# Kernel optimization log

Measured on AMD Instinct MI355X. Metric: run time of the kernel, lower is better.

## Reference

```python
import jax, jax.numpy as jnp
import numpy as np

D = 768       # GATv2 in/out feats (num_heads=1)
D_OUT = 384   # fc output
K = 51        # round(top_rate * L) = round(0.1 * 512)
EPS = 1e-5    # nn.LayerNorm default eps


def _layer_norm(x, g, b):
    mu = jnp.mean(x, axis=-1, keepdims=True)
    var = jnp.mean((x - mu) ** 2, axis=-1, keepdims=True)
    return (x - mu) / jnp.sqrt(var + EPS) * g + b


def setup_inputs() -> dict:
    key = jax.random.key(0)
    ks = jax.random.split(key, 12)
    B, L = 4, 512
    s = 0.02
    return {
        "hidden_state": jax.random.normal(ks[0], (B, L, D), jnp.float32),
        "attention": jax.random.uniform(ks[1], (B, L, L), jnp.float32),
        # GATv2Conv params (fc_src, fc_dst, attn vector, output bias)
        "W_src": jax.random.normal(ks[2], (D, D), jnp.float32) * s,
        "b_src": jnp.zeros((D,), jnp.float32),
        "W_dst": jax.random.normal(ks[3], (D, D), jnp.float32) * s,
        "b_dst": jnp.zeros((D,), jnp.float32),
        "attn_vec": jax.random.normal(ks[4], (D,), jnp.float32) * s,
        "gat_bias": jnp.zeros((D,), jnp.float32),
        # GlobalAttentionPooling gate_nn: Linear(768, 1)
        "gate_W": jax.random.normal(ks[5], (D, 1), jnp.float32) * s,
        "gate_b": jnp.zeros((1,), jnp.float32),
        # LayerNorm(768)
        "ln_g": jnp.ones((D,), jnp.float32),
        "ln_b": jnp.zeros((D,), jnp.float32),
        # fc: Linear(768, 384)
        "fc_W": jax.random.normal(ks[6], (D, D_OUT), jnp.float32) * s,
        "fc_b": jnp.zeros((D_OUT,), jnp.float32),
        # LayerNorm(384)
        "ln2_g": jnp.ones((D_OUT,), jnp.float32),
        "ln2_b": jnp.zeros((D_OUT,), jnp.float32),
        "mask": jnp.ones((B, L), jnp.int32),  # unused by the original forward
        "type": 0,                              # unused string/type flag
    }


def reference(hidden_state, attention, W_src, b_src, W_dst, b_dst, attn_vec,
              gat_bias, gate_W, gate_b, ln_g, ln_b, fc_W, fc_b, ln2_g, ln2_b,
              mask, type):
    B, L, _ = hidden_state.shape
    # --- topk sparsification: each node i keeps K source neighbors ---
    vals, idx = jax.lax.top_k(attention, K)          # [B, L, K]
    valid = vals > 0.0                                # edges kept by pos_sign filter

    # --- GATv2Conv (num_heads=1, residual=Identity since 768==768) ---
    feat_src = hidden_state @ W_src + b_src           # [B, L, D]
    feat_dst = hidden_state @ W_dst + b_dst           # [B, L, D]
    g = feat_src[jnp.arange(B)[:, None, None], idx]   # [B, L, K, D] gathered src feats
    e = jax.nn.leaky_relu(g + feat_dst[:, :, None, :], 0.2)
    scores = jnp.einsum("blkd,d->blk", e, attn_vec)   # [B, L, K]
    scores = jnp.where(valid, scores, -1e9)           # removed edges masked out
    a = jax.nn.softmax(scores, axis=-1)               # edge_softmax per dst node
    h = jnp.einsum("blk,blkd->bld", a, g)             # weighted scatter-sum
    h = h + hidden_state + gat_bias                   # residual (identity) + bias
    h = jax.nn.leaky_relu(h, 0.01)                    # nn.LeakyReLU activation

    # --- GlobalAttentionPooling: softmax(gate) weighted segment reduce ---
    gate = h @ gate_W + gate_b                        # [B, L, 1]
    p = jax.nn.softmax(gate, axis=1)
    pooled = jnp.sum(p * h, axis=1)                   # [B, D]

    # --- head: fc(dropout(ln(relu(out)))) then ln2 (dropout = eval identity) ---
    out = _layer_norm(jax.nn.relu(pooled), ln_g, ln_b)
    out = out @ fc_W + fc_b
    out = _layer_norm(out, ln2_g, ln2_b)
    return out
```

## Files before the change

kernel.cpp:

```cpp
#include <hip/hip_runtime.h>
#include <math.h>

#define D 768
#define DOUT 384
#define LSEQ 512
#define BATCH 4
#define KTOP 51
#define EPS 1e-5f

typedef unsigned short ushort_t;
typedef __bf16 bf16x8 __attribute__((ext_vector_type(8)));
typedef float f32x4 __attribute__((ext_vector_type(4)));

#define GLOAD16(gp, lp)                                                        \
    __builtin_amdgcn_global_load_lds(                                          \
        (const __attribute__((address_space(1))) unsigned int*)(gp),           \
        (__attribute__((address_space(3))) unsigned int*)(lp), 16, 0, 0)

__device__ __forceinline__ ushort_t f2bf(float f) {
    unsigned int u = __builtin_bit_cast(unsigned int, f);
    u = (u + 0x7FFFu + ((u >> 16) & 1u)) >> 16;
    return (ushort_t)u;
}

__device__ __forceinline__ float bf2f(ushort_t u) {
    unsigned int v = ((unsigned int)u) << 16;
    return __builtin_bit_cast(float, v);
}

__global__ __launch_bounds__(256) void prep_kernel(const float* __restrict__ hidden,
                                                   ushort_t* __restrict__ Ah,
                                                   const float* __restrict__ W0,
                                                   const float* __restrict__ W1,
                                                   ushort_t* __restrict__ WT0,
                                                   ushort_t* __restrict__ WT1,
                                                   float* __restrict__ pooled,
                                                   float* __restrict__ z) {
    __shared__ float tile[32][33];
    const int bid = blockIdx.x;
    const int tid = threadIdx.x;
    if (bid < 1536) {
        const int i = (bid * 256 + tid) * 4;
        const float4 v = *(const float4*)(hidden + i);
        ushort4 o;
        o.x = f2bf(v.x); o.y = f2bf(v.y); o.z = f2bf(v.z); o.w = f2bf(v.w);
        *(ushort4*)(Ah + i) = o;
    } else if (bid < 2688) {
        const int t = bid - 1536;
        const int zz = t / 576;
        const int rem = t - zz * 576;
        const int by = rem / 24, bx = rem - by * 24;
        const float* W = zz ? W1 : W0;
        ushort_t* WT = zz ? WT1 : WT0;
        const int kbase = by * 32;
        const int nbase = bx * 32;
        const int r = tid >> 3, c4 = (tid & 7) * 4;

        const float4 v = *(const float4*)(W + (size_t)(kbase + r) * D + nbase + c4);
        tile[r][c4 + 0] = v.x; tile[r][c4 + 1] = v.y;
        tile[r][c4 + 2] = v.z; tile[r][c4 + 3] = v.w;
        __syncthreads();
        ushort4 o;
        o.x = f2bf(tile[c4 + 0][r]); o.y = f2bf(tile[c4 + 1][r]);
        o.z = f2bf(tile[c4 + 2][r]); o.w = f2bf(tile[c4 + 3][r]);
        *(ushort4*)(WT + (size_t)(nbase + r) * D + kbase + c4) = o;
    } else {
        for (int i = tid; i < BATCH * D; i += 256) pooled[i] = 0.f;
        for (int i = tid; i < BATCH * DOUT; i += 256) z[i] = 0.f;
    }
}

__global__ __launch_bounds__(256) void feat_gemm_kernel(const ushort_t* __restrict__ Ah,
                                                        const ushort_t* __restrict__ WT0,
                                                        const float* __restrict__ b0,
                                                        ushort_t* __restrict__ Csrc_bf,
                                                        const ushort_t* __restrict__ WT1,
                                                        const float* __restrict__ b1,
                                                        float* __restrict__ Cdst) {
    const ushort_t* WT = blockIdx.z ? WT1 : WT0;
    const float* bias = blockIdx.z ? b1 : b0;

    __shared__ ushort_t As[64 * 32];
    __shared__ ushort_t Bs[64 * 32];

    const int tid = threadIdx.x;
    const int lane = tid & 63;
    const int wave = tid >> 6;
    const int quad = lane >> 4;
    const int m15 = lane & 15;
    const int qRow = (wave & 1) * 32;
    const int qCol = (wave >> 1) * 32;

    const int rowBase = blockIdx.y * 64;
    const int colBase = blockIdx.x * 64;

    const int e0 = tid * 8;
    const int r0 = e0 >> 5;
    const int c0 = e0 & 31;
    const ushort_t* Abase = Ah + (size_t)rowBase * D;
    const ushort_t* Bbase = WT + (size_t)colBase * D;

    f32x4 acc[2][2] = {};

    for (int kk = 0; kk < D; kk += 32) {
        __syncthreads();
        GLOAD16(Abase + (size_t)r0 * D + kk + c0, &As[e0]);
        GLOAD16(Bbase + (size_t)r0 * D + kk + c0, &Bs[e0]);
        __syncthreads();

        bf16x8 a[2], b[2];
#pragma unroll
        for (int i = 0; i < 2; ++i)
            a[i] = *(const bf16x8*)&As[(qRow + i * 16 + m15) * 32 + quad * 8];
#pragma unroll
        for (int j = 0; j < 2; ++j)
            b[j] = *(const bf16x8*)&Bs[(qCol + j * 16 + m15) * 32 + quad * 8];
#pragma unroll
        for (int i = 0; i < 2; ++i)
#pragma unroll
            for (int j = 0; j < 2; ++j)
                acc[i][j] = __builtin_amdgcn_mfma_f32_16x16x32_bf16(a[i], b[j], acc[i][j], 0, 0, 0);
    }

    if (blockIdx.z == 0) {
#pragma unroll
        for (int j = 0; j < 2; ++j) {
            const int col = colBase + qCol + j * 16 + m15;
            const float bv = bias[col];
#pragma unroll
            for (int i = 0; i < 2; ++i) {
                ushort_t* Cp = Csrc_bf + (size_t)(rowBase + qRow + i * 16 + quad * 4) * D + col;
#pragma unroll
                for (int r = 0; r < 4; ++r)
                    Cp[(size_t)r * D] = f2bf(acc[i][j][r] + bv);
            }
        }
    } else {
#pragma unroll
        for (int j = 0; j < 2; ++j) {
            const int col = colBase + qCol + j * 16 + m15;
            const float bv = bias[col];
#pragma unroll
            for (int i = 0; i < 2; ++i) {
                float* Cp = Cdst + (size_t)(rowBase + qRow + i * 16 + quad * 4) * D + col;
#pragma unroll
                for (int r = 0; r < 4; ++r)
                    Cp[(size_t)r * D] = acc[i][j][r] + bv;
            }
        }
    }
}

__global__ __launch_bounds__(256) void transpose_fsrc_kernel(const ushort_t* __restrict__ I,
                                                             ushort_t* __restrict__ O) {
    __shared__ ushort_t tile[32][33];
    const int b = blockIdx.z;
    const int cbase = blockIdx.x * 32;
    const int rbase = blockIdx.y * 32;
    const int tid = threadIdx.x;
    const int tr = tid >> 3, tc4 = (tid & 7) * 4;

    const ushort_t* Ib = I + (size_t)b * LSEQ * D;
    ushort_t* Ob = O + (size_t)b * D * LSEQ;

    const ushort4 v = *(const ushort4*)(Ib + (size_t)(rbase + tr) * D + cbase + tc4);
    tile[tr][tc4 + 0] = v.x; tile[tr][tc4 + 1] = v.y;
    tile[tr][tc4 + 2] = v.z; tile[tr][tc4 + 3] = v.w;
    __syncthreads();
    ushort4 o;
    o.x = tile[tc4 + 0][tr]; o.y = tile[tc4 + 1][tr];
    o.z = tile[tc4 + 2][tr]; o.w = tile[tc4 + 3][tr];
    *(ushort4*)(Ob + (size_t)(cbase + tr) * LSEQ + rbase + tc4) = o;
}

__global__ __launch_bounds__(256) void score_kernel(const float* __restrict__ attn,
                                                    const ushort_t* __restrict__ fsrc_bf,
                                                    const float* __restrict__ feat_dst,
                                                    const float* __restrict__ attn_vec,
                                                    const float* __restrict__ gate_b,
                                                    ushort_t* __restrict__ P,
                                                    float* __restrict__ gate) {
    const int row = blockIdx.x;
    const int b = row >> 9;
    const int tid = threadIdx.x;
    const int lane = tid & 63;
    const int wave = tid >> 6;

    __shared__ float vals[LSEQ];
    __shared__ float cval[320];
    __shared__ int   cidx[320];
    __shared__ int   nhi, outSlot;
    __shared__ float sc[KTOP];
    __shared__ int   kid[KTOP];
    __shared__ float kvv[KTOP];

    ((unsigned int*)(P + (size_t)row * LSEQ))[tid] = 0u;
    if (tid == 0) { gate[row] = gate_b[0]; nhi = 0; outSlot = 0; }

    const float* a = attn + (size_t)row * LSEQ;
    const float v0 = a[tid];
    const float v1 = a[tid + 256];
    vals[tid] = v0;
    vals[tid + 256] = v1;
    __syncthreads();

    if (v0 > 0.75f) {
        const int s = atomicAdd(&nhi, 1);
        if (s < 320) { cval[s] = v0; cidx[s] = tid; }
    }
    if (v1 > 0.75f) {
        const int s = atomicAdd(&nhi, 1);
        if (s < 320) { cval[s] = v1; cidx[s] = tid + 256; }
    }
    __syncthreads();

    const int n = nhi;
    if (n >= KTOP && n <= 320) {
        if (tid < n) {
            const float v = cval[tid];
            const int e = cidx[tid];
            int r = 0;
            for (int j = 0; j < n; ++j) {
                const float u = cval[j];
                r += (u > v) || (u == v && cidx[j] < e);
            }
            if (r < KTOP) {
                const int s = atomicAdd(&outSlot, 1);
                kid[s] = e; kvv[s] = v;
            }
        }
    } else {
#pragma unroll
        for (int e0 = 0; e0 < 2; ++e0) {
            const int e = tid + e0 * 256;
            const float v = vals[e];
            int r = 0;
            for (int j = 0; j < LSEQ; ++j) {
                const float u = vals[j];
                r += (u > v) || (u == v && j < e);
            }
            if (r < KTOP) {
                const int s = atomicAdd(&outSlot, 1);
                kid[s] = e; kvv[s] = v;
            }
        }
    }

    const float* fdp = feat_dst + (size_t)row * D;
    float fdr[16], avr[16];
    {
        const int d0 = lane * 8;
        const float4 f0 = *(const float4*)(fdp + d0);
        const float4 f1 = *(const float4*)(fdp + d0 + 4);
        const float4 a0 = *(const float4*)(attn_vec + d0);
        const float4 a1 = *(const float4*)(attn_vec + d0 + 4);
        fdr[0]=f0.x; fdr[1]=f0.y; fdr[2]=f0.z; fdr[3]=f0.w;
        fdr[4]=f1.x; fdr[5]=f1.y; fdr[6]=f1.z; fdr[7]=f1.w;
        avr[0]=a0.x; avr[1]=a0.y; avr[2]=a0.z; avr[3]=a0.w;
        avr[4]=a1.x; avr[5]=a1.y; avr[6]=a1.z; avr[7]=a1.w;
    }
    if (lane < 32) {
        const int d1 = (lane + 64) * 8;
        const float4 f0 = *(const float4*)(fdp + d1);
        const float4 f1 = *(const float4*)(fdp + d1 + 4);
        const float4 a0 = *(const float4*)(attn_vec + d1);
        const float4 a1 = *(const float4*)(attn_vec + d1 + 4);
        fdr[8]=f0.x; fdr[9]=f0.y; fdr[10]=f0.z; fdr[11]=f0.w;
        fdr[12]=f1.x; fdr[13]=f1.y; fdr[14]=f1.z; fdr[15]=f1.w;
        avr[8]=a0.x; avr[9]=a0.y; avr[10]=a0.z; avr[11]=a0.w;
        avr[12]=a1.x; avr[13]=a1.y; avr[14]=a1.z; avr[15]=a1.w;
    }
    __syncthreads();

    for (int k = wave; k < KTOP; k += 4) {
        const ushort_t* g = fsrc_bf + ((size_t)(b << 9) + kid[k]) * D;
        float s = 0.f;
        const bf16x8 g0 = *(const bf16x8*)(g + lane * 8);
#pragma unroll
        for (int jj = 0; jj < 8; ++jj) {
            float x = (float)g0[jj] + fdr[jj];
            x = x > 0.f ? x : 0.2f * x;
            s += x * avr[jj];
        }
        if (lane < 32) {
            const bf16x8 g1 = *(const bf16x8*)(g + (lane + 64) * 8);
#pragma unroll
            for (int jj = 0; jj < 8; ++jj) {
                float x = (float)g1[jj] + fdr[8 + jj];
                x = x > 0.f ? x : 0.2f * x;
                s += x * avr[8 + jj];
            }
        }
#pragma unroll
        for (int off = 32; off > 0; off >>= 1) s += __shfl_down(s, off);
        if (lane == 0) sc[k] = (kvv[k] > 0.f) ? s : -1e9f;
    }
    __syncthreads();

    if (wave == 0) {
        float s = (lane < KTOP) ? sc[lane] : -3.0e38f;
        float m = s;
#pragma unroll
        for (int off = 32; off > 0; off >>= 1) m = fmaxf(m, __shfl_xor(m, off));
        float e = (lane < KTOP) ? __expf(s - m) : 0.f;
        float sum = e;
#pragma unroll
        for (int off = 32; off > 0; off >>= 1) sum += __shfl_xor(sum, off);
        if (lane < KTOP) sc[lane] = e / sum;
    }
    __syncthreads();

    if (tid < KTOP)
        P[(size_t)row * LSEQ + kid[tid]] = f2bf(sc[tid]);
}

__global__ __launch_bounds__(256) void pgemm_kernel(const ushort_t* __restrict__ P,
                                                    const ushort_t* __restrict__ fsrcT,
                                                    const float* __restrict__ gat_bias,
                                                    const float* __restrict__ hidden,
                                                    const float* __restrict__ gate_W,
                                                    ushort_t* __restrict__ h,
                                                    float* __restrict__ gate) {
    const int bb = blockIdx.z;
    const ushort_t* Ab = P + (size_t)bb * LSEQ * LSEQ;
    const ushort_t* Bb = fsrcT + (size_t)bb * D * LSEQ;

    __shared__ ushort_t As[64 * 32];
    __shared__ ushort_t Bs[64 * 32];

    const int tid = threadIdx.x;
    const int lane = tid & 63;
    const int wave = tid >> 6;
    const int quad = lane >> 4;
    const int m15 = lane & 15;
    const int qRow = (wave & 1) * 32;
    const int qCol = (wave >> 1) * 32;

    const int rowBase = blockIdx.y * 64;
    const int colBase = blockIdx.x * 64;

    const int e0 = tid * 8;
    const int r0 = e0 >> 5;
    const int c0 = e0 & 31;
    const ushort_t* Abase = Ab + (size_t)rowBase * LSEQ;
    const ushort_t* Bbase = Bb + (size_t)colBase * LSEQ;

    f32x4 acc[2][2] = {};

    for (int kk = 0; kk < LSEQ; kk += 32) {
        __syncthreads();
        GLOAD16(Abase + (size_t)r0 * LSEQ + kk + c0, &As[e0]);
        GLOAD16(Bbase + (size_t)r0 * LSEQ + kk + c0, &Bs[e0]);
        __syncthreads();

        bf16x8 a[2], b[2];
#pragma unroll
        for (int i = 0; i < 2; ++i)
            a[i] = *(const bf16x8*)&As[(qRow + i * 16 + m15) * 32 + quad * 8];
#pragma unroll
        for (int j = 0; j < 2; ++j)
            b[j] = *(const bf16x8*)&Bs[(qCol + j * 16 + m15) * 32 + quad * 8];
#pragma unroll
        for (int i = 0; i < 2; ++i)
#pragma unroll
            for (int j = 0; j < 2; ++j)
                acc[i][j] = __builtin_amdgcn_mfma_f32_16x16x32_bf16(a[i], b[j], acc[i][j], 0, 0, 0);
    }

    const float* hidb = hidden + (size_t)bb * LSEQ * D;
    ushort_t* hb = h + (size_t)bb * LSEQ * D;
    float rp[2][4] = {};
#pragma unroll
    for (int j = 0; j < 2; ++j) {
        const int col = colBase + qCol + j * 16 + m15;
        const float bv = gat_bias[col];
        const float gw = gate_W[col];
#pragma unroll
        for (int i = 0; i < 2; ++i) {
            const int row0 = rowBase + qRow + i * 16 + quad * 4;
#pragma unroll
            for (int r = 0; r < 4; ++r) {
                float v = acc[i][j][r] + bv + hidb[(size_t)(row0 + r) * D + col];
                v = v > 0.f ? v : 0.01f * v;
                hb[(size_t)(row0 + r) * D + col] = f2bf(v);
                rp[i][r] += v * gw;
            }
        }
    }
#pragma unroll
    for (int i = 0; i < 2; ++i)
#pragma unroll
        for (int r = 0; r < 4; ++r) {
            float p4 = rp[i][r];
            p4 += __shfl_xor(p4, 1);
            p4 += __shfl_xor(p4, 2);
            p4 += __shfl_xor(p4, 4);
            p4 += __shfl_xor(p4, 8);
            if (m15 == 0)
                atomicAdd(&gate[bb * LSEQ + rowBase + qRow + i * 16 + quad * 4 + r], p4);
        }
}

__global__ __launch_bounds__(256) void pool_kernel(const ushort_t* __restrict__ h,
                                                   const float* __restrict__ gate,
                                                   float* __restrict__ pooled) {
    const int b = blockIdx.z;
    const int lbase = blockIdx.y * 64;
    const int d = blockIdx.x * 256 + threadIdx.x;
    const int tid = threadIdx.x;

    __shared__ float red[256];
    __shared__ float ps[64];

    const float g0 = gate[b * LSEQ + tid];
    const float g1 = gate[b * LSEQ + tid + 256];
    red[tid] = fmaxf(g0, g1);
    __syncthreads();
    for (int s = 128; s > 0; s >>= 1) { if (tid < s) red[tid] = fmaxf(red[tid], red[tid + s]); __syncthreads(); }
    const float m = red[0];
    __syncthreads();
    red[tid] = __expf(g0 - m) + __expf(g1 - m);
    __syncthreads();
    for (int s = 128; s > 0; s >>= 1) { if (tid < s) red[tid] += red[tid + s]; __syncthreads(); }
    const float inv = 1.f / red[0];
    if (tid < 64) ps[tid] = __expf(gate[b * LSEQ + lbase + tid] - m) * inv;
    __syncthreads();

    const ushort_t* hb = h + ((size_t)(b * LSEQ + lbase)) * D + d;
    float acc = 0.f;
#pragma unroll 8
    for (int l = 0; l < 64; ++l) {
        acc += ps[l] * bf2f(hb[(size_t)l * D]);
    }
    atomicAdd(&pooled[b * D + d], acc);
}

__global__ __launch_bounds__(256) void fc_kernel(const float* __restrict__ pooled,
                                                 const float* __restrict__ ln_g,
                                                 const float* __restrict__ ln_b,
                                                 const float* __restrict__ fc_W,
                                                 float* __restrict__ z) {
    const int b = blockIdx.z;
    const int by = blockIdx.y;
    const int dbase = by * 256;
    const int jbase = blockIdx.x * 64;
    const int tid = threadIdx.x;
    const int jt = tid & 63;
    const int sub = tid >> 6;

    __shared__ float red[256];
    __shared__ float ys[256];
    __shared__ float part[4][64];

    float v[3];
#pragma unroll
    for (int i = 0; i < 3; ++i) v[i] = fmaxf(pooled[b * D + tid + i * 256], 0.f);

    red[tid] = v[0] + v[1] + v[2];
    __syncthreads();
    for (int s = 128; s > 0; s >>= 1) { if (tid < s) red[tid] += red[tid + s]; __syncthreads(); }
    const float mu = red[0] / (float)D;
    __syncthreads();
    float vs = 0.f;
#pragma unroll
    for (int i = 0; i < 3; ++i) { const float dd = v[i] - mu; vs += dd * dd; }
    red[tid] = vs;
    __syncthreads();
    for (int s = 128; s > 0; s >>= 1) { if (tid < s) red[tid] += red[tid + s]; __syncthreads(); }
    const float rstd = rsqrtf(red[0] / (float)D + EPS);

    const float vb = (by == 0) ? v[0] : (by == 1 ? v[1] : v[2]);
    ys[tid] = (vb - mu) * rstd * ln_g[dbase + tid] + ln_b[dbase + tid];
    __syncthreads();

    const float* W = fc_W + (size_t)(dbase + sub * 64) * DOUT + jbase + jt;
    const float* yy = ys + sub * 64;
    float acc = 0.f;
#pragma unroll 8
    for (int i = 0; i < 64; ++i) {
        acc += yy[i] * W[(size_t)i * DOUT];
    }
    part[sub][jt] = acc;
    __syncthreads();
    if (sub == 0) {
        const float tot = part[0][jt] + part[1][jt] + part[2][jt] + part[3][jt];
        atomicAdd(&z[b * DOUT + jbase + jt], tot);
    }
}

__global__ __launch_bounds__(384) void ln2_kernel(const float* __restrict__ z,
                                                  const float* __restrict__ fc_b,
                                                  const float* __restrict__ ln2_g,
                                                  const float* __restrict__ ln2_b,
                                                  float* __restrict__ out) {
    const int b = blockIdx.x;
    const int tid = threadIdx.x;
    const int lane = tid & 63;
    const int wave = tid >> 6;
    __shared__ float wred[6];

    const float v = z[b * DOUT + tid] + fc_b[tid];

    float s = v;
#pragma unroll
    for (int off = 32; off > 0; off >>= 1) s += __shfl_xor(s, off);
    if (lane == 0) wred[wave] = s;
    __syncthreads();
    float mu = 0.f;
#pragma unroll
    for (int w = 0; w < 6; ++w) mu += wred[w];
    mu /= (float)DOUT;
    __syncthreads();

    const float dd = v - mu;
    float s2 = dd * dd;
#pragma unroll
    for (int off = 32; off > 0; off >>= 1) s2 += __shfl_xor(s2, off);
    if (lane == 0) wred[wave] = s2;
    __syncthreads();
    float var = 0.f;
#pragma unroll
    for (int w = 0; w < 6; ++w) var += wred[w];
    const float rstd = rsqrtf(var / (float)DOUT + EPS);

    out[b * DOUT + tid] = dd * rstd * ln2_g[tid] + ln2_b[tid];
}

extern "C" void kernel_launch(void* const* d_in, const int* in_sizes, int n_in,
                              void* d_out, int out_size, void* d_ws, size_t ws_size,
                              hipStream_t stream) {
    const float* hidden   = (const float*)d_in[0];
    const float* attention= (const float*)d_in[1];
    const float* W_src    = (const float*)d_in[2];
    const float* b_src    = (const float*)d_in[3];
    const float* W_dst    = (const float*)d_in[4];
    const float* b_dst    = (const float*)d_in[5];
    const float* attn_vec = (const float*)d_in[6];
    const float* gat_bias = (const float*)d_in[7];
    const float* gate_W   = (const float*)d_in[8];
    const float* gate_b   = (const float*)d_in[9];
    const float* ln_g     = (const float*)d_in[10];
    const float* ln_b     = (const float*)d_in[11];
    const float* fc_W     = (const float*)d_in[12];
    const float* fc_b     = (const float*)d_in[13];
    const float* ln2_g    = (const float*)d_in[14];
    const float* ln2_b    = (const float*)d_in[15];
    float* out = (float*)d_out;

    const int M = BATCH * LSEQ;
    float* feat_dst = (float*)d_ws;
    float* gate     = feat_dst + (size_t)M * D;
    float* pooled   = gate + M;
    float* z        = pooled + BATCH * D;
    ushort_t* Ah    = (ushort_t*)(z + BATCH * DOUT);
    ushort_t* WT0   = Ah + (size_t)M * D;
    ushort_t* WT1   = WT0 + (size_t)D * D;
    ushort_t* fsrcb = WT1 + (size_t)D * D;
    ushort_t* fsrcT = fsrcb + (size_t)M * D;
    ushort_t* P     = fsrcT + (size_t)M * D;
    ushort_t* h     = P + (size_t)M * LSEQ;

    hipLaunchKernelGGL(prep_kernel, dim3(2689), dim3(256), 0, stream,
                       hidden, Ah, W_src, W_dst, WT0, WT1, pooled, z);
    hipLaunchKernelGGL(feat_gemm_kernel, dim3(D / 64, M / 64, 2), dim3(256), 0, stream,
                       Ah, WT0, b_src, fsrcb, WT1, b_dst, feat_dst);
    hipLaunchKernelGGL(transpose_fsrc_kernel, dim3(D / 32, LSEQ / 32, BATCH), dim3(256), 0, stream,
                       fsrcb, fsrcT);
    hipLaunchKernelGGL(score_kernel, dim3(M), dim3(256), 0, stream,
                       attention, fsrcb, feat_dst, attn_vec, gate_b, P, gate);
    hipLaunchKernelGGL(pgemm_kernel, dim3(D / 64, LSEQ / 64, BATCH), dim3(256), 0, stream,
                       P, fsrcT, gat_bias, hidden, gate_W, h, gate);
    hipLaunchKernelGGL(pool_kernel, dim3(D / 256, LSEQ / 64, BATCH), dim3(256), 0, stream,
                       h, gate, pooled);
    hipLaunchKernelGGL(fc_kernel, dim3(DOUT / 64, D / 256, BATCH), dim3(256), 0, stream,
                       pooled, ln_g, ln_b, fc_W, z);
    hipLaunchKernelGGL(ln2_kernel, dim3(BATCH), dim3(384), 0, stream,
                       z, fc_b, ln2_g, ln2_b, out);
}
```

Measured before the change: 176.6 us.

## Replace dense P-GEMM aggregation with sparse top-k gather kernel and swizzle feat GEMM

The edge aggregation used to scatter softmax weights into a dense 512x512 bf16 P matrix per batch, transpose feat_src, and run a dense GEMM. It now stores the 51 (prob, index) pairs per row and uses a per-row wave gather kernel that sums the weighted bf16 source rows directly and fuses residual, bias, LeakyReLU and the gate dot. This removes the transpose kernel, the P zeroing, the dense GEMM and the gate atomics. The feature GEMM also moves to a 64-wide K tile with an XOR-swizzled LDS layout, and the block reductions in the pool and fc kernels switch to wave shuffles. The gather does irregular row reads that depend on L2 hit rates.

```diff
diff --git a/kernel.cpp b/kernel.cpp
--- a/kernel.cpp
+++ b/kernel.cpp
@@ -80,8 +80,8 @@
     const ushort_t* WT = blockIdx.z ? WT1 : WT0;
     const float* bias = blockIdx.z ? b1 : b0;
 
-    __shared__ ushort_t As[64 * 32];
-    __shared__ ushort_t Bs[64 * 32];
+    __shared__ ushort_t As[64 * 64];
+    __shared__ ushort_t Bs[64 * 64];
 
     const int tid = threadIdx.x;
     const int lane = tid & 63;
@@ -95,31 +95,47 @@
     const int colBase = blockIdx.x * 64;
 
     const int e0 = tid * 8;
-    const int r0 = e0 >> 5;
-    const int c0 = e0 & 31;
+    const int r0 = e0 >> 6;
+    const int c0 = e0 & 63;
+    const int cc = c0 >> 3;
+    const int csw = (cc ^ (r0 & 7)) << 3;
     const ushort_t* Abase = Ah + (size_t)rowBase * D;
     const ushort_t* Bbase = WT + (size_t)colBase * D;
 
     f32x4 acc[2][2] = {};
 
-    for (int kk = 0; kk < D; kk += 32) {
+    for (int kk = 0; kk < D; kk += 64) {
         __syncthreads();
-        GLOAD16(Abase + (size_t)r0 * D + kk + c0, &As[e0]);
-        GLOAD16(Bbase + (size_t)r0 * D + kk + c0, &Bs[e0]);
+        GLOAD16(Abase + (size_t)r0 * D + kk + csw, &As[e0]);
+        GLOAD16(Abase + (size_t)(r0 + 32) * D + kk + csw, &As[e0 + 2048]);
+        GLOAD16(Bbase + (size_t)r0 * D + kk + csw, &Bs[e0]);
+        GLOAD16(Bbase + (size_t)(r0 + 32) * D + kk + csw, &Bs[e0 + 2048]);
         __syncthreads();
 
-        bf16x8 a[2], b[2];
-#pragma unroll
-        for (int i = 0; i < 2; ++i)
-            a[i] = *(const bf16x8*)&As[(qRow + i * 16 + m15) * 32 + quad * 8];
-#pragma unroll
-        for (int j = 0; j < 2; ++j)
-            b[j] = *(const bf16x8*)&Bs[(qCol + j * 16 + m15) * 32 + quad * 8];
-#pragma unroll
-        for (int i = 0; i < 2; ++i)
-#pragma unroll
-            for (int j = 0; j < 2; ++j)
-                acc[i][j] = __builtin_amdgcn_mfma_f32_16x16x32_bf16(a[i], b[j], acc[i][j], 0, 0, 0);
+        bf16x8 a[2][2], b[2][2];
+#pragma unroll
+        for (int i = 0; i < 2; ++i) {
+            const int row = qRow + i * 16 + m15;
+            const int sw = row & 7;
+#pragma unroll
+            for (int ks = 0; ks < 2; ++ks)
+                a[i][ks] = *(const bf16x8*)&As[row * 64 + ((((ks << 2) + quad) ^ sw) << 3)];
+        }
+#pragma unroll
+        for (int j = 0; j < 2; ++j) {
+            const int row = qCol + j * 16 + m15;
+            const int sw = row & 7;
+#pragma unroll
+            for (int ks = 0; ks < 2; ++ks)
+                b[j][ks] = *(const bf16x8*)&Bs[row * 64 + ((((ks << 2) + quad) ^ sw) << 3)];
+        }
+#pragma unroll
+        for (int ks = 0; ks < 2; ++ks)
+#pragma unroll
+            for (int i = 0; i < 2; ++i)
+#pragma unroll
+                for (int j = 0; j < 2; ++j)
+                    acc[i][j] = __builtin_amdgcn_mfma_f32_16x16x32_bf16(a[i][ks], b[j][ks], acc[i][j], 0, 0, 0);
     }
 
     if (blockIdx.z == 0) {
@@ -149,37 +165,14 @@
             }
         }
     }
-}
-
-__global__ __launch_bounds__(256) void transpose_fsrc_kernel(const ushort_t* __restrict__ I,
-                                                             ushort_t* __restrict__ O) {
-    __shared__ ushort_t tile[32][33];
-    const int b = blockIdx.z;
-    const int cbase = blockIdx.x * 32;
-    const int rbase = blockIdx.y * 32;
-    const int tid = threadIdx.x;
-    const int tr = tid >> 3, tc4 = (tid & 7) * 4;
-
-    const ushort_t* Ib = I + (size_t)b * LSEQ * D;
-    ushort_t* Ob = O + (size_t)b * D * LSEQ;
-
-    const ushort4 v = *(const ushort4*)(Ib + (size_t)(rbase + tr) * D + cbase + tc4);
-    tile[tr][tc4 + 0] = v.x; tile[tr][tc4 + 1] = v.y;
-    tile[tr][tc4 + 2] = v.z; tile[tr][tc4 + 3] = v.w;
-    __syncthreads();
-    ushort4 o;
-    o.x = tile[tc4 + 0][tr]; o.y = tile[tc4 + 1][tr];
-    o.z = tile[tc4 + 2][tr]; o.w = tile[tc4 + 3][tr];
-    *(ushort4*)(Ob + (size_t)(cbase + tr) * LSEQ + rbase + tc4) = o;
 }
 
 __global__ __launch_bounds__(256) void score_kernel(const float* __restrict__ attn,
                                                     const ushort_t* __restrict__ fsrc_bf,
                                                     const float* __restrict__ feat_dst,
                                                     const float* __restrict__ attn_vec,
-                                                    const float* __restrict__ gate_b,
-                                                    ushort_t* __restrict__ P,
-                                                    float* __restrict__ gate) {
+                                                    float* __restrict__ kprob,
+                                                    int* __restrict__ kidx) {
     const int row = blockIdx.x;
     const int b = row >> 9;
     const int tid = threadIdx.x;
@@ -194,8 +187,7 @@
     __shared__ int   kid[KTOP];
     __shared__ float kvv[KTOP];
 
-    ((unsigned int*)(P + (size_t)row * LSEQ))[tid] = 0u;
-    if (tid == 0) { gate[row] = gate_b[0]; nhi = 0; outSlot = 0; }
+    if (tid == 0) { nhi = 0; outSlot = 0; }
 
     const float* a = attn + (size_t)row * LSEQ;
     const float v0 = a[tid];
@@ -310,95 +302,92 @@
     }
     __syncthreads();
 
-    if (tid < KTOP)
-        P[(size_t)row * LSEQ + kid[tid]] = f2bf(sc[tid]);
-}
-
-__global__ __launch_bounds__(256) void pgemm_kernel(const ushort_t* __restrict__ P,
-                                                    const ushort_t* __restrict__ fsrcT,
-                                                    const float* __restrict__ gat_bias,
-                                                    const float* __restrict__ hidden,
-                                                    const float* __restrict__ gate_W,
-                                                    ushort_t* __restrict__ h,
-                                                    float* __restrict__ gate) {
-    const int bb = blockIdx.z;
-    const ushort_t* Ab = P + (size_t)bb * LSEQ * LSEQ;
-    const ushort_t* Bb = fsrcT + (size_t)bb * D * LSEQ;
-
-    __shared__ ushort_t As[64 * 32];
-    __shared__ ushort_t Bs[64 * 32];
-
-    const int tid = threadIdx.x;
-    const int lane = tid & 63;
-    const int wave = tid >> 6;
-    const int quad = lane >> 4;
-    const int m15 = lane & 15;
-    const int qRow = (wave & 1) * 32;
-    const int qCol = (wave >> 1) * 32;
-
-    const int rowBase = blockIdx.y * 64;
-    const int colBase = blockIdx.x * 64;
-
-    const int e0 = tid * 8;
-    const int r0 = e0 >> 5;
-    const int c0 = e0 & 31;
-    const ushort_t* Abase = Ab + (size_t)rowBase * LSEQ;
-    const ushort_t* Bbase = Bb + (size_t)colBase * LSEQ;
-
-    f32x4 acc[2][2] = {};
-
-    for (int kk = 0; kk < LSEQ; kk += 32) {
-        __syncthreads();
-        GLOAD16(Abase + (size_t)r0 * LSEQ + kk + c0, &As[e0]);
-        GLOAD16(Bbase + (size_t)r0 * LSEQ + kk + c0, &Bs[e0]);
-        __syncthreads();
-
-        bf16x8 a[2], b[2];
-#pragma unroll
-        for (int i = 0; i < 2; ++i)
-            a[i] = *(const bf16x8*)&As[(qRow + i * 16 + m15) * 32 + quad * 8];
-#pragma unroll
-        for (int j = 0; j < 2; ++j)
-            b[j] = *(const bf16x8*)&Bs[(qCol + j * 16 + m15) * 32 + quad * 8];
-#pragma unroll
-        for (int i = 0; i < 2; ++i)
-#pragma unroll
-            for (int j = 0; j < 2; ++j)
-                acc[i][j] = __builtin_amdgcn_mfma_f32_16x16x32_bf16(a[i], b[j], acc[i][j], 0, 0, 0);
-    }
-
-    const float* hidb = hidden + (size_t)bb * LSEQ * D;
-    ushort_t* hb = h + (size_t)bb * LSEQ * D;
-    float rp[2][4] = {};
-#pragma unroll
-    for (int j = 0; j < 2; ++j) {
-        const int col = colBase + qCol + j * 16 + m15;
-        const float bv = gat_bias[col];
-        const float gw = gate_W[col];
-#pragma unroll
-        for (int i = 0; i < 2; ++i) {
-            const int row0 = rowBase + qRow + i * 16 + quad * 4;
-#pragma unroll
-            for (int r = 0; r < 4; ++r) {
-                float v = acc[i][j][r] + bv + hidb[(size_t)(row0 + r) * D + col];
-                v = v > 0.f ? v : 0.01f * v;
-                hb[(size_t)(row0 + r) * D + col] = f2bf(v);
-                rp[i][r] += v * gw;
-            }
-        }
-    }
-#pragma unroll
-    for (int i = 0; i < 2; ++i)
-#pragma unroll
-        for (int r = 0; r < 4; ++r) {
-            float p4 = rp[i][r];
-            p4 += __shfl_xor(p4, 1);
-            p4 += __shfl_xor(p4, 2);
-            p4 += __shfl_xor(p4, 4);
-            p4 += __shfl_xor(p4, 8);
-            if (m15 == 0)
-                atomicAdd(&gate[bb * LSEQ + rowBase + qRow + i * 16 + quad * 4 + r], p4);
-        }
+    if (tid < KTOP) {
+        kprob[(size_t)row * 64 + tid] = sc[tid];
+        kidx[(size_t)row * 64 + tid]  = kid[tid];
+    }
+}
+
+__global__ __launch_bounds__(256) void gath_kernel(const float* __restrict__ kprob,
+                                                   const int* __restrict__ kidx,
+                                                   const ushort_t* __restrict__ fsrc,
+                                                   const float* __restrict__ gat_bias,
+                                                   const float* __restrict__ hidden,
+                                                   const float* __restrict__ gate_W,
+                                                   const float* __restrict__ gate_b,
+                                                   ushort_t* __restrict__ h,
+                                                   float* __restrict__ gate) {
+    const int w = threadIdx.x >> 6;
+    const int lane = threadIdx.x & 63;
+    const int row = blockIdx.x * 4 + w;
+    const int b = row >> 9;
+
+    __shared__ float ps[4][KTOP];
+    __shared__ int   is_[4][KTOP];
+    if (lane < KTOP) {
+        ps[w][lane]  = kprob[(size_t)row * 64 + lane];
+        is_[w][lane] = kidx[(size_t)row * 64 + lane];
+    }
+    __syncthreads();
+
+    const int d0 = lane * 8;
+    const int d1 = 512 + lane * 4;
+    const ushort_t* fb = fsrc + ((size_t)(b << 9)) * D;
+
+    float acc[12] = {};
+    for (int k = 0; k < KTOP; ++k) {
+        const float p = ps[w][k];
+        const ushort_t* g = fb + (size_t)is_[w][k] * D;
+        const bf16x8 g0 = *(const bf16x8*)(g + d0);
+        const ushort4 g1 = *(const ushort4*)(g + d1);
+#pragma unroll
+        for (int jj = 0; jj < 8; ++jj) acc[jj] += p * (float)g0[jj];
+        acc[8]  += p * bf2f(g1.x);
+        acc[9]  += p * bf2f(g1.y);
+        acc[10] += p * bf2f(g1.z);
+        acc[11] += p * bf2f(g1.w);
+    }
+
+    const float* hid = hidden + (size_t)row * D;
+    const float4 h0 = *(const float4*)(hid + d0);
+    const float4 h1 = *(const float4*)(hid + d0 + 4);
+    const float4 h2 = *(const float4*)(hid + d1);
+    const float4 b0 = *(const float4*)(gat_bias + d0);
+    const float4 b1 = *(const float4*)(gat_bias + d0 + 4);
+    const float4 b2 = *(const float4*)(gat_bias + d1);
+    const float4 w0 = *(const float4*)(gate_W + d0);
+    const float4 w1 = *(const float4*)(gate_W + d0 + 4);
+    const float4 w2 = *(const float4*)(gate_W + d1);
+
+    float v[12], gw[12];
+    v[0]=acc[0]+h0.x+b0.x; v[1]=acc[1]+h0.y+b0.y; v[2]=acc[2]+h0.z+b0.z; v[3]=acc[3]+h0.w+b0.w;
+    v[4]=acc[4]+h1.x+b1.x; v[5]=acc[5]+h1.y+b1.y; v[6]=acc[6]+h1.z+b1.z; v[7]=acc[7]+h1.w+b1.w;
+    v[8]=acc[8]+h2.x+b2.x; v[9]=acc[9]+h2.y+b2.y; v[10]=acc[10]+h2.z+b2.z; v[11]=acc[11]+h2.w+b2.w;
+    gw[0]=w0.x; gw[1]=w0.y; gw[2]=w0.z; gw[3]=w0.w;
+    gw[4]=w1.x; gw[5]=w1.y; gw[6]=w1.z; gw[7]=w1.w;
+    gw[8]=w2.x; gw[9]=w2.y; gw[10]=w2.z; gw[11]=w2.w;
+
+    float dot = 0.f;
+#pragma unroll
+    for (int jj = 0; jj < 12; ++jj) {
+        float x = v[jj];
+        x = x > 0.f ? x : 0.01f * x;
+        v[jj] = x;
+        dot += x * gw[jj];
+    }
+
+    ushort_t* hb = h + (size_t)row * D;
+    ushort4 o;
+    o.x = f2bf(v[0]); o.y = f2bf(v[1]); o.z = f2bf(v[2]); o.w = f2bf(v[3]);
+    *(ushort4*)(hb + d0) = o;
+    o.x = f2bf(v[4]); o.y = f2bf(v[5]); o.z = f2bf(v[6]); o.w = f2bf(v[7]);
+    *(ushort4*)(hb + d0 + 4) = o;
+    o.x = f2bf(v[8]); o.y = f2bf(v[9]); o.z = f2bf(v[10]); o.w = f2bf(v[11]);
+    *(ushort4*)(hb + d1) = o;
+
+#pragma unroll
+    for (int off = 32; off > 0; off >>= 1) dot += __shfl_down(dot, off);
+    if (lane == 0) gate[row] = gate_b[0] + dot;
 }
 
 __global__ __launch_bounds__(256) void pool_kernel(const ushort_t* __restrict__ h,
@@ -408,21 +397,27 @@
     const int lbase = blockIdx.y * 64;
     const int d = blockIdx.x * 256 + threadIdx.x;
     const int tid = threadIdx.x;
-
-    __shared__ float red[256];
+    const int lane = tid & 63;
+    const int w = tid >> 6;
+
+    __shared__ float wred[4];
     __shared__ float ps[64];
 
     const float g0 = gate[b * LSEQ + tid];
     const float g1 = gate[b * LSEQ + tid + 256];
-    red[tid] = fmaxf(g0, g1);
-    __syncthreads();
-    for (int s = 128; s > 0; s >>= 1) { if (tid < s) red[tid] = fmaxf(red[tid], red[tid + s]); __syncthreads(); }
-    const float m = red[0];
-    __syncthreads();
-    red[tid] = __expf(g0 - m) + __expf(g1 - m);
-    __syncthreads();
-    for (int s = 128; s > 0; s >>= 1) { if (tid < s) red[tid] += red[tid + s]; __syncthreads(); }
-    const float inv = 1.f / red[0];
+    float m = fmaxf(g0, g1);
+#pragma unroll
+    for (int off = 32; off > 0; off >>= 1) m = fmaxf(m, __shfl_xor(m, off));
+    if (lane == 0) wred[w] = m;
+    __syncthreads();
+    m = fmaxf(fmaxf(wred[0], wred[1]), fmaxf(wred[2], wred[3]));
+    float e = __expf(g0 - m) + __expf(g1 - m);
+#pragma unroll
+    for (int off = 32; off > 0; off >>= 1) e += __shfl_xor(e, off);
+    __syncthreads();
+    if (lane == 0) wred[w] = e;
+    __syncthreads();
+    const float inv = 1.f / (wred[0] + wred[1] + wred[2] + wred[3]);
     if (tid < 64) ps[tid] = __expf(gate[b * LSEQ + lbase + tid] - m) * inv;
     __syncthreads();
 
@@ -445,10 +440,12 @@
     const int dbase = by * 256;
     const int jbase = blockIdx.x * 64;
     const int tid = threadIdx.x;
+    const int lane = tid & 63;
+    const int w = tid >> 6;
     const int jt = tid & 63;
     const int sub = tid >> 6;
 
-    __shared__ float red[256];
+    __shared__ float wred[4];
     __shared__ float ys[256];
     __shared__ float part[4][64];
 
@@ -456,18 +453,21 @@
 #pragma unroll
     for (int i = 0; i < 3; ++i) v[i] = fmaxf(pooled[b * D + tid + i * 256], 0.f);
 
-    red[tid] = v[0] + v[1] + v[2];
-    __syncthreads();
-    for (int s = 128; s > 0; s >>= 1) { if (tid < s) red[tid] += red[tid + s]; __syncthreads(); }
-    const float mu = red[0] / (float)D;
-    __syncthreads();
+    float s = v[0] + v[1] + v[2];
+#pragma unroll
+    for (int off = 32; off > 0; off >>= 1) s += __shfl_xor(s, off);
+    if (lane == 0) wred[w] = s;
+    __syncthreads();
+    const float mu = (wred[0] + wred[1] + wred[2] + wred[3]) / (float)D;
     float vs = 0.f;
 #pragma unroll
     for (int i = 0; i < 3; ++i) { const float dd = v[i] - mu; vs += dd * dd; }
-    red[tid] = vs;
-    __syncthreads();
-    for (int s = 128; s > 0; s >>= 1) { if (tid < s) red[tid] += red[tid + s]; __syncthreads(); }
-    const float rstd = rsqrtf(red[0] / (float)D + EPS);
+#pragma unroll
+    for (int off = 32; off > 0; off >>= 1) vs += __shfl_xor(vs, off);
+    __syncthreads();
+    if (lane == 0) wred[w] = vs;
+    __syncthreads();
+    const float rstd = rsqrtf((wred[0] + wred[1] + wred[2] + wred[3]) / (float)D + EPS);
 
     const float vb = (by == 0) ? v[0] : (by == 1 ? v[1] : v[2]);
     ys[tid] = (vb - mu) * rstd * ln_g[dbase + tid] + ln_b[dbase + tid];
@@ -552,24 +552,22 @@
     float* gate     = feat_dst + (size_t)M * D;
     float* pooled   = gate + M;
     float* z        = pooled + BATCH * D;
-    ushort_t* Ah    = (ushort_t*)(z + BATCH * DOUT);
+    float* kprob    = z + BATCH * DOUT;
+    int*   kidx     = (int*)(kprob + (size_t)M * 64);
+    ushort_t* Ah    = (ushort_t*)(kidx + (size_t)M * 64);
     ushort_t* WT0   = Ah + (size_t)M * D;
     ushort_t* WT1   = WT0 + (size_t)D * D;
     ushort_t* fsrcb = WT1 + (size_t)D * D;
-    ushort_t* fsrcT = fsrcb + (size_t)M * D;
-    ushort_t* P     = fsrcT + (size_t)M * D;
-    ushort_t* h     = P + (size_t)M * LSEQ;
+    ushort_t* h     = fsrcb + (size_t)M * D;
 
     hipLaunchKernelGGL(prep_kernel, dim3(2689), dim3(256), 0, stream,
                        hidden, Ah, W_src, W_dst, WT0, WT1, pooled, z);
     hipLaunchKernelGGL(feat_gemm_kernel, dim3(D / 64, M / 64, 2), dim3(256), 0, stream,
                        Ah, WT0, b_src, fsrcb, WT1, b_dst, feat_dst);
-    hipLaunchKernelGGL(transpose_fsrc_kernel, dim3(D / 32, LSEQ / 32, BATCH), dim3(256), 0, stream,
-                       fsrcb, fsrcT);
     hipLaunchKernelGGL(score_kernel, dim3(M), dim3(256), 0, stream,
-                       attention, fsrcb, feat_dst, attn_vec, gate_b, P, gate);
-    hipLaunchKernelGGL(pgemm_kernel, dim3(D / 64, LSEQ / 64, BATCH), dim3(256), 0, stream,
-                       P, fsrcT, gat_bias, hidden, gate_W, h, gate);
+                       attention, fsrcb, feat_dst, attn_vec, kprob, kidx);
+    hipLaunchKernelGGL(gath_kernel, dim3(M / 4), dim3(256), 0, stream,
+                       kprob, kidx, fsrcb, gat_bias, hidden, gate_W, gate_b, h, gate);
     hipLaunchKernelGGL(pool_kernel, dim3(D / 256, LSEQ / 64, BATCH), dim3(256), 0, stream,
                        h, gate, pooled);
     hipLaunchKernelGGL(fc_kernel, dim3(DOUT / 64, D / 256, BATCH), dim3(256), 0, stream,
```

Measured after the change: 172.4 us. -2.4%, faster.
